# Optimization experiments

Measured on AMD Instinct MI355X. Metric: run time of the kernel, lower is better.

The kernel has to match this reference:

```python
import jax, jax.numpy as jnp
import numpy as np

S, B, D, F = 2048, 8, 1024, 4096
EPS = 1e-5

def setup_inputs() -> dict:
    key = jax.random.key(0)
    ks = jax.random.split(key, 16)
    sc = lambda fan_in: 1.0 / np.sqrt(fan_in)
    inp = {
        'src': jax.random.normal(ks[0], (S, B, D), dtype=jnp.float32),
        'wq': jax.random.uniform(ks[1], (D, D), jnp.float32, -sc(D), sc(D)),
        'bq': jnp.zeros((D,), jnp.float32),
        'wk': jax.random.uniform(ks[2], (D, D), jnp.float32, -sc(D), sc(D)),
        'bk': jnp.zeros((D,), jnp.float32),
        'wv': jax.random.uniform(ks[3], (D, D), jnp.float32, -sc(D), sc(D)),
        'bv': jnp.zeros((D,), jnp.float32),
        'wo': jax.random.uniform(ks[4], (D, D), jnp.float32, -sc(D), sc(D)),
        'bo': jnp.zeros((D,), jnp.float32),
        'w1': jax.random.uniform(ks[5], (F, D), jnp.float32, -sc(D), sc(D)),
        'b1': jnp.zeros((F,), jnp.float32),
        'w2': jax.random.uniform(ks[6], (D, F), jnp.float32, -sc(F), sc(F)),
        'b2': jnp.zeros((D,), jnp.float32),
        'g1': jnp.ones((D,), jnp.float32),
        'be1': jnp.zeros((D,), jnp.float32),
        'g2': jnp.ones((D,), jnp.float32),
        'be2': jnp.zeros((D,), jnp.float32),
    }
    return inp

def _layer_norm(x, g, b):
    mu = jnp.mean(x, axis=-1, keepdims=True)
    var = jnp.mean(jnp.square(x - mu), axis=-1, keepdims=True)
    return (x - mu) / jnp.sqrt(var + EPS) * g + b

def _forward(src, wq, bq, wk, bk, wv, bv, wo, bo, w1, b1, w2, b2, g1, be1, g2, be2):
    # Linear attention (ELU+1 feature map, no normalizer — faithful to source)
    Q = jax.nn.elu(src @ wq.T + bq) + 1.0  # [S,B,D]
    K = jax.nn.elu(src @ wk.T + bk) + 1.0  # [S,B,D]
    V = src @ wv.T + bv                    # [S,B,D]
    KV = jnp.einsum('sbd,sbe->bde', K, V)  # [B,D,D]
    attn = jnp.einsum('sbd,bde->sbe', Q, KV)  # [S,B,D]
    attn = attn @ wo.T + bo
    x = _layer_norm(src + attn, g1, be1)   # dropout is identity (p=0 / eval)
    ffn = jax.nn.relu(x @ w1.T + b1) @ w2.T + b2
    return _layer_norm(x + ffn, g2, be2)

def reference(src, wq, bq, wk, bk, wv, bv, wo, bo, w1, b1, w2, b2, g1, be1, g2, be2):
    return _forward(src, wq, bq, wk, bk, wv, bv, wo, bo, w1, b1, w2, b2, g1, be1, g2, be2)
```

## Files before the change

kernel.cpp:

```cpp
#include <hip/hip_runtime.h>
#include <hip/hip_bf16.h>
#include <math.h>


typedef __attribute__((ext_vector_type(8))) short short8;
typedef __attribute__((ext_vector_type(4))) short short4_t;
typedef __attribute__((ext_vector_type(4))) float f32x4;

#define S_DIM 2048
#define B_DIM 8
#define D_DIM 1024
#define F_DIM 4096

__device__ __forceinline__ unsigned short f2bf(float f) {
  __hip_bfloat16 h = __float2bfloat16(f);
  return *reinterpret_cast<unsigned short*>(&h);
}

#define GLD16(gp, sp)                                              \
  __builtin_amdgcn_global_load_lds(                                \
      (const __attribute__((address_space(1))) void*)(gp),         \
      (__attribute__((address_space(3))) void*)(sp), 16, 0, 0)

#define BAR()                                  \
  do {                                         \
    asm volatile("" ::: "memory");             \
    __builtin_amdgcn_s_barrier();              \
    asm volatile("" ::: "memory");             \
  } while (0)
#define WAITVM6() asm volatile("s_waitcnt vmcnt(6)" ::: "memory")
#define WAITVM10() asm volatile("s_waitcnt vmcnt(10)" ::: "memory")
#define WAITVM0() asm volatile("s_waitcnt vmcnt(0)" ::: "memory")
#define LGKM0_FENCE()                                        \
  do {                                                       \
    asm volatile("s_waitcnt lgkmcnt(0)" ::: "memory");       \
    __builtin_amdgcn_sched_barrier(0);                       \
  } while (0)

template <int EPI>
__global__ __launch_bounds__(512, 2) void gemm256_kernel(
    const unsigned short* __restrict__ A, long lda, long sA,
    const unsigned short* __restrict__ B, long ldb, long sB,
    void* __restrict__ Cv, long ldc, long sC,
    const float* __restrict__ bias,
    const float* __restrict__ resid, long ldr, long sR, int K) {
  __shared__ short lds[65536];
  const int gx = gridDim.x;
  const int nwg = gx * gridDim.y;
  const int orig = blockIdx.y * gx + blockIdx.x;
  const int cpx = nwg >> 3;
  const int wgid = (orig & 7) * cpx + (orig >> 3);
  const int bx = wgid % gx, by = wgid / gx;
  const int bz = blockIdx.z;
  const unsigned short* Ablk = A + (long)bz * sA + (long)by * 256 * lda;
  const unsigned short* Bblk = B + (long)bz * sB + (long)bx * 256 * ldb;

  const int tid = threadIdx.x;
  const int w = tid >> 6, lane = tid & 63;
  const int wm = w >> 2, wn = w & 3;
  const int lr = lane & 15, kh = lane >> 4;

  const int sr = w * 8 + (lane >> 3);
  const int sc = ((lane & 7) ^ (lane >> 3)) * 8;
  const int br0 = sr + ((sr >> 5) << 5);
  const unsigned short* pA = Ablk + (long)sr * lda + sc;
  const unsigned short* pB = Bblk + (long)br0 * ldb + sc;
  const long dA1 = 128 * lda, dAh = 64 * lda;
  const long dB1 = 128 * ldb, dBh = 32 * ldb;
  const int dst0 = w * 1024;
  const int dst1 = (8 + w) * 1024;

#define STAGE_A(bufOff, h, rel)                                               \
  do {                                                                        \
    GLD16(pA + (h) * dAh + (rel) * 64,                                        \
          (char*)lds + (bufOff) + (h)*16384 + dst0);                          \
    GLD16(pA + (h) * dAh + dA1 + (rel) * 64,                                  \
          (char*)lds + (bufOff) + (h)*16384 + dst1);                          \
  } while (0)
#define STAGE_B(bufOff, nh, rel)                                              \
  do {                                                                        \
    GLD16(pB + (nh) * dBh + (rel) * 64,                                       \
          (char*)lds + (bufOff) + 32768 + (nh)*16384 + dst0);                 \
    GLD16(pB + (nh) * dBh + dB1 + (rel) * 64,                                 \
          (char*)lds + (bufOff) + 32768 + (nh)*16384 + dst1);                 \
  } while (0)

  const int chk0 = ((kh ^ (lr & 7)) << 4);
  const int chk1 = (((4 + kh) ^ (lr & 7)) << 4);
  const int aRdBase = (wm * 64 + lr) * 128;
  const int bRdBase = (wn * 32 + lr) * 128;

  short8 af[4][2], b0r[2][2], b1r[2][2];
  f32x4 acc[8][4];
#pragma unroll
  for (int m = 0; m < 8; ++m)
#pragma unroll
    for (int n = 0; n < 4; ++n)
#pragma unroll
      for (int j = 0; j < 4; ++j) acc[m][n][j] = 0.f;

#define LDA_H(bufOff, h)                                                     \
  do {                                                                       \
    const char* _p = (const char*)lds + (bufOff) + (h)*16384 + aRdBase;      \
    _Pragma("unroll") for (int m = 0; m < 4; ++m) {                          \
      af[m][0] = *(const short8*)(_p + m * 2048 + chk0);                     \
      af[m][1] = *(const short8*)(_p + m * 2048 + chk1);                     \
    }                                                                        \
  } while (0)
#define LDB_H(dst, bufOff, nh)                                               \
  do {                                                                       \
    const char* _p = (const char*)lds + (bufOff) + 32768 + (nh)*16384 + bRdBase; \
    _Pragma("unroll") for (int n = 0; n < 2; ++n) {                          \
      dst[n][0] = *(const short8*)(_p + n * 2048 + chk0);                    \
      dst[n][1] = *(const short8*)(_p + n * 2048 + chk1);                    \
    }                                                                        \
  } while (0)
#define MFMA_Q(mh, nh, bset)                                                 \
  do {                                                                       \
    __builtin_amdgcn_s_setprio(1);                                           \
    _Pragma("unroll") for (int m = 0; m < 4; ++m)                            \
    _Pragma("unroll") for (int n = 0; n < 2; ++n)                            \
    _Pragma("unroll") for (int ks = 0; ks < 2; ++ks)                         \
      acc[(mh)*4 + m][(nh)*2 + n] = __builtin_amdgcn_mfma_f32_16x16x32_bf16( \
          af[m][ks], bset[n][ks], acc[(mh)*4 + m][(nh)*2 + n], 0, 0, 0);     \
    __builtin_amdgcn_s_setprio(0);                                           \
  } while (0)

  const int T = K >> 6;
  STAGE_A(0, 0, 0); STAGE_B(0, 0, 0); STAGE_B(0, 1, 0); STAGE_A(0, 1, 0);
  STAGE_A(65536, 0, 1); STAGE_B(65536, 0, 1); STAGE_B(65536, 1, 1);
  WAITVM10(); BAR();
  LDB_H(b0r, 0, 0);

  for (int i = 0; i < (T >> 1) - 1; ++i) {
    LDA_H(0, 0); STAGE_A(65536, 1, 1);
    BAR(); LGKM0_FENCE(); MFMA_Q(0, 0, b0r); BAR();
    LDB_H(b1r, 0, 1); STAGE_A(0, 0, 2);
    BAR(); LGKM0_FENCE(); MFMA_Q(0, 1, b1r); BAR();
    LDA_H(0, 1); STAGE_B(0, 0, 2);
    BAR(); LGKM0_FENCE(); MFMA_Q(1, 1, b1r); BAR();
    STAGE_B(0, 1, 2);
    WAITVM6(); BAR(); MFMA_Q(1, 0, b0r); LDB_H(b0r, 65536, 0); BAR();
    LDA_H(65536, 0); STAGE_A(0, 1, 2);
    BAR(); LGKM0_FENCE(); MFMA_Q(0, 0, b0r); BAR();
    LDB_H(b1r, 65536, 1); STAGE_A(65536, 0, 3);
    BAR(); LGKM0_FENCE(); MFMA_Q(0, 1, b1r); BAR();
    LDA_H(65536, 1); STAGE_B(65536, 0, 3);
    BAR(); LGKM0_FENCE(); MFMA_Q(1, 1, b1r); BAR();
    STAGE_B(65536, 1, 3);
    WAITVM6(); BAR(); MFMA_Q(1, 0, b0r); LDB_H(b0r, 0, 0); BAR();
    pA += 128; pB += 128;
  }

  LDA_H(0, 0); STAGE_A(65536, 1, 1);
  BAR(); LGKM0_FENCE(); MFMA_Q(0, 0, b0r); BAR();
  LDB_H(b1r, 0, 1);
  BAR(); LGKM0_FENCE(); MFMA_Q(0, 1, b1r); BAR();
  LDA_H(0, 1);
  BAR(); LGKM0_FENCE(); MFMA_Q(1, 1, b1r); BAR();
  WAITVM0(); BAR(); MFMA_Q(1, 0, b0r); LDB_H(b0r, 65536, 0); BAR();
  LDA_H(65536, 0);
  BAR(); LGKM0_FENCE(); MFMA_Q(0, 0, b0r); BAR();
  LDB_H(b1r, 65536, 1);
  BAR(); LGKM0_FENCE(); MFMA_Q(0, 1, b1r); BAR();
  LDA_H(65536, 1);
  BAR(); LGKM0_FENCE(); MFMA_Q(1, 1, b1r); BAR();
  LGKM0_FENCE(); MFMA_Q(1, 0, b0r);

  const long gm0 = (long)by * 256 + wm * 128;
  const long gn0 = (long)bx * 256 + wn * 64;
  if constexpr (EPI == 4) {
    float* C = (float*)Cv + (long)bz * sC;
    const float* R = resid + (long)bz * sR;
#pragma unroll
    for (int mg = 0; mg < 8; ++mg)
#pragma unroll
      for (int ng = 0; ng < 4; ++ng) {
        const long col = gn0 + ng * 16 + lr;
        const float bcol = bias[col];
#pragma unroll
        for (int j = 0; j < 4; ++j) {
          const long row = gm0 + mg * 16 + kh * 4 + j;
          C[row * ldc + col] = acc[mg][ng][j] + bcol + R[row * ldr + col];
        }
      }
  } else {
    unsigned short* C = (unsigned short*)Cv + (long)bz * sC;
    const bool do_elu = (EPI == 5) && (gn0 < 2048);
#pragma unroll
    for (int mg = 0; mg < 8; ++mg)
#pragma unroll
      for (int ng = 0; ng < 4; ++ng) {
        const long col = gn0 + ng * 16 + lr;
        const float bcol = bias[col];
#pragma unroll
        for (int j = 0; j < 4; ++j) {
          const long row = gm0 + mg * 16 + kh * 4 + j;
          float v = acc[mg][ng][j] + bcol;
          if constexpr (EPI == 3) v = fmaxf(v, 0.f);
          if constexpr (EPI == 5) {
            if (do_elu) v = (v > 0.f) ? (v + 1.f) : expf(v);
          }
          C[row * ldc + col] = f2bf(v);
        }
      }
  }
#undef STAGE_A
#undef STAGE_B
#undef LDA_H
#undef LDB_H
#undef MFMA_Q
}

template <int EPI>
__global__ __launch_bounds__(256, 2) void gemm_bt_kernel(
    const unsigned short* __restrict__ A, long lda, long sA,
    const unsigned short* __restrict__ B, long ldb, long sB,
    void* __restrict__ Cv, long ldc, long sC,
    const float* __restrict__ bias,
    const float* __restrict__ resid, long ldr, long sR, int K) {
  __shared__ short As[128 * 32];
  __shared__ short Bs[128 * 32];
  const int gx = gridDim.x;
  const int nwg = gx * gridDim.y;
  const int orig = blockIdx.y * gx + blockIdx.x;
  const int cpx = nwg >> 3;
  const int wgid = (orig & 7) * cpx + (orig >> 3);
  const int bx = wgid % gx;
  const int by = wgid / gx;

  const int bz = blockIdx.z;
  const unsigned short* Ab = A + (long)bz * sA + (long)by * 128 * lda;
  const unsigned short* Bb = B + (long)bz * sB + (long)bx * 128 * ldb;
  const int tid = threadIdx.x;
  const int w = tid >> 6, lane = tid & 63;
  const int srow = lane >> 2;
  const int scol = (lane & 3) * 8;
  const int wr = (w >> 1) * 64, wc = (w & 1) * 64;
  const int lr = lane & 15, kh = lane >> 4;

  f32x4 acc[4][4];
#pragma unroll
  for (int m = 0; m < 4; ++m)
#pragma unroll
    for (int n = 0; n < 4; ++n)
#pragma unroll
      for (int j = 0; j < 4; ++j) acc[m][n][j] = 0.f;

  const unsigned short* ga0 = Ab + (long)(w * 16 + srow) * lda + scol;
  const unsigned short* ga1 = Ab + (long)(64 + w * 16 + srow) * lda + scol;
  const unsigned short* gb0 = Bb + (long)(w * 16 + srow) * ldb + scol;
  const unsigned short* gb1 = Bb + (long)(64 + w * 16 + srow) * ldb + scol;
  short* la0 = &As[(w * 16) * 32];
  short* la1 = &As[(64 + w * 16) * 32];
  short* lb0 = &Bs[(w * 16) * 32];
  short* lb1 = &Bs[(64 + w * 16) * 32];

  for (int k0 = 0; k0 < K; k0 += 32) {
    GLD16(ga0 + k0, la0);
    GLD16(ga1 + k0, la1);
    GLD16(gb0 + k0, lb0);
    GLD16(gb1 + k0, lb1);
    __syncthreads();
    short8 af[4], bf[4];
#pragma unroll
    for (int m = 0; m < 4; ++m)
      af[m] = *(const short8*)&As[(wr + m * 16 + lr) * 32 + kh * 8];
#pragma unroll
    for (int n = 0; n < 4; ++n)
      bf[n] = *(const short8*)&Bs[(wc + n * 16 + lr) * 32 + kh * 8];
#pragma unroll
    for (int m = 0; m < 4; ++m)
#pragma unroll
      for (int n = 0; n < 4; ++n)
        acc[m][n] =
            __builtin_amdgcn_mfma_f32_16x16x32_bf16(af[m], bf[n], acc[m][n], 0, 0, 0);
    __syncthreads();
  }

  const long gm0 = (long)by * 128 + wr;
  const long gn0 = (long)bx * 128 + wc;
  unsigned short* C = (unsigned short*)Cv + (long)bz * sC;
#pragma unroll
  for (int m = 0; m < 4; ++m)
#pragma unroll
    for (int n = 0; n < 4; ++n) {
      const long col = gn0 + n * 16 + lr;
#pragma unroll
      for (int j = 0; j < 4; ++j) {
        const long row = gm0 + m * 16 + kh * 4 + j;
        C[row * ldc + col] = f2bf(acc[m][n][j]);
      }
    }
}

__global__ __launch_bounds__(256) void transpose_kernel(
    const unsigned short* __restrict__ in, unsigned short* __restrict__ out,
    long ld) {
  __shared__ unsigned short t[64][68];
  const int b = blockIdx.z;
  const long s0 = (long)blockIdx.x * 64, d0 = (long)blockIdx.y * 64;
  const int tid = threadIdx.x;
  {
    const int r = tid >> 3, c = (tid & 7) * 8;
#pragma unroll
    for (int it = 0; it < 2; ++it) {
      const int s = r + it * 32;
      const unsigned short* g = &in[((s0 + s) * B_DIM + b) * ld + d0 + c];
      short4_t v0 = *(const short4_t*)g;
      short4_t v1 = *(const short4_t*)(g + 4);
      *(short4_t*)&t[s][c] = v0;
      *(short4_t*)&t[s][c + 4] = v1;
    }
  }
  __syncthreads();
  {
    const int d = tid >> 3, c = (tid & 7) * 8;
#pragma unroll
    for (int it = 0; it < 2; ++it) {
      const int dd = d + it * 32;
      short8 v;
#pragma unroll
      for (int j = 0; j < 8; ++j) v[j] = (short)t[c + j][dd];
      *(short8*)&out[(long)b * ((long)D_DIM * S_DIM) + (d0 + dd) * S_DIM + s0 + c] = v;
    }
  }
}

template <int WRITE_BF16>
__global__ __launch_bounds__(256) void layernorm_kernel(
    const float* in, float* outf, unsigned short* __restrict__ outb,
    const float* __restrict__ gamma, const float* __restrict__ beta) {
  const long row = blockIdx.x;
  const float* x = in + row * D_DIM;
  const int tid = threadIdx.x;
  const int lane = tid & 63, w = tid >> 6;
  f32x4 v = *(const f32x4*)&x[tid * 4];
  float s = v[0] + v[1] + v[2] + v[3];
  float q = v[0] * v[0] + v[1] * v[1] + v[2] * v[2] + v[3] * v[3];
#pragma unroll
  for (int off = 32; off > 0; off >>= 1) {
    s += __shfl_down(s, off, 64);
    q += __shfl_down(q, off, 64);
  }
  __shared__ float red[8];
  if (lane == 0) { red[w] = s; red[w + 4] = q; }
  __syncthreads();
  s = red[0] + red[1] + red[2] + red[3];
  q = red[4] + red[5] + red[6] + red[7];
  const float mu = s * (1.f / D_DIM);
  const float var = q * (1.f / D_DIM) - mu * mu;
  const float rs = rsqrtf(var + 1e-5f);
  f32x4 g = *(const f32x4*)&gamma[tid * 4];
  f32x4 bb = *(const f32x4*)&beta[tid * 4];
  f32x4 o;
#pragma unroll
  for (int j = 0; j < 4; ++j) o[j] = (v[j] - mu) * rs * g[j] + bb[j];
  *(f32x4*)&outf[row * D_DIM + tid * 4] = o;
  if constexpr (WRITE_BF16) {
    short4_t ob;
#pragma unroll
    for (int j = 0; j < 4; ++j) ob[j] = (short)f2bf(o[j]);
    *(short4_t*)&outb[row * D_DIM + tid * 4] = ob;
  }
}

__global__ __launch_bounds__(256) void cast_kernel(
    const float* __restrict__ in, unsigned short* __restrict__ out, long n) {
  long i = ((long)blockIdx.x * 256 + threadIdx.x) * 8;
  if (i >= n) return;
  f32x4 a = *(const f32x4*)&in[i];
  f32x4 b = *(const f32x4*)&in[i + 4];
  short8 v;
#pragma unroll
  for (int j = 0; j < 4; ++j) v[j] = (short)f2bf(a[j]);
#pragma unroll
  for (int j = 0; j < 4; ++j) v[4 + j] = (short)f2bf(b[j]);
  *(short8*)&out[i] = v;
}

extern "C" void kernel_launch(void* const* d_in, const int* in_sizes, int n_in,
                              void* d_out, int out_size, void* d_ws, size_t ws_size,
                              hipStream_t stream) {
  const float* src = (const float*)d_in[0];
  const float* wq  = (const float*)d_in[1];
  const float* bq  = (const float*)d_in[2];
  const float* wk  = (const float*)d_in[3];
  const float* bk  = (const float*)d_in[4];
  const float* wv  = (const float*)d_in[5];
  const float* bv  = (const float*)d_in[6];
  const float* wo  = (const float*)d_in[7];
  const float* bo  = (const float*)d_in[8];
  const float* w1  = (const float*)d_in[9];
  const float* b1  = (const float*)d_in[10];
  const float* w2  = (const float*)d_in[11];
  const float* b2  = (const float*)d_in[12];
  const float* g1  = (const float*)d_in[13];
  const float* be1 = (const float*)d_in[14];
  const float* g2  = (const float*)d_in[15];
  const float* be2 = (const float*)d_in[16];

  const long MB = 1024L * 1024L;
  if (ws_size < 248 * MB) return;
  char* ws = (char*)d_ws;
  unsigned short* w1b   = (unsigned short*)(ws + 0 * MB);
  unsigned short* w2b   = (unsigned short*)(ws + 8 * MB);
  unsigned short* srcb  = (unsigned short*)(ws + 16 * MB);
  unsigned short* Kt    = (unsigned short*)(ws + 16 * MB);
  unsigned short* Vt    = (unsigned short*)(ws + 48 * MB);
  float*          AO    = (float*)(ws + 16 * MB);
  float*          X     = (float*)(ws + 16 * MB);
  unsigned short* KVm   = (unsigned short*)(ws + 80 * MB);
  unsigned short* Mt    = (unsigned short*)(ws + 96 * MB);
  unsigned short* Xb    = (unsigned short*)(ws + 80 * MB);
  unsigned short* wqkvb = (unsigned short*)(ws + 112 * MB);
  float*          bqkv  = (float*)(ws + 118 * MB);
  unsigned short* wob   = (unsigned short*)(ws + 119 * MB);
  unsigned short* QKVb  = (unsigned short*)(ws + 144 * MB);
  unsigned short* H     = (unsigned short*)(ws + 112 * MB);

  const dim3 blk(256);
  const dim3 blk512(512);
  cast_kernel<<<dim3(512), blk, 0, stream>>>(wq, wqkvb, 1048576);
  cast_kernel<<<dim3(512), blk, 0, stream>>>(wk, wqkvb + 1048576, 1048576);
  cast_kernel<<<dim3(512), blk, 0, stream>>>(wv, wqkvb + 2097152, 1048576);
  cast_kernel<<<dim3(512), blk, 0, stream>>>(wo, wob, 1048576);
  cast_kernel<<<dim3(2048), blk, 0, stream>>>(w1, w1b, 4194304);
  cast_kernel<<<dim3(2048), blk, 0, stream>>>(w2, w2b, 4194304);
  cast_kernel<<<dim3(8192), blk, 0, stream>>>(src, srcb, 16777216);
  hipMemcpyAsync(bqkv, bq, 4096, hipMemcpyDeviceToDevice, stream);
  hipMemcpyAsync(bqkv + 1024, bk, 4096, hipMemcpyDeviceToDevice, stream);
  hipMemcpyAsync(bqkv + 2048, bv, 4096, hipMemcpyDeviceToDevice, stream);

  gemm256_kernel<5><<<dim3(12, 64, 1), blk512, 0, stream>>>(
      srcb, 1024, 0, wqkvb, 1024, 0, QKVb, 3072, 0, bqkv, nullptr, 0, 0, 1024);

  transpose_kernel<<<dim3(32, 16, 8), blk, 0, stream>>>(QKVb + 1024, Kt, 3072);
  transpose_kernel<<<dim3(32, 16, 8), blk, 0, stream>>>(QKVb + 2048, Vt, 3072);

  gemm_bt_kernel<0><<<dim3(8, 8, 8), blk, 0, stream>>>(
      Kt, 2048, 2097152, Vt, 2048, 2097152, KVm, 1024, 1048576,
      nullptr, nullptr, 0, 0, 2048);
  gemm_bt_kernel<0><<<dim3(8, 8, 8), blk, 0, stream>>>(
      wob, 1024, 0, KVm, 1024, 1048576, Mt, 1024, 1048576,
      nullptr, nullptr, 0, 0, 1024);
  gemm256_kernel<4><<<dim3(4, 8, 8), blk512, 0, stream>>>(
      QKVb, 24576, 3072, Mt, 1024, 1048576, AO, 8192, 1024,
      bo, src, 8192, 1024, 1024);

  layernorm_kernel<1><<<dim3(16384), blk, 0, stream>>>(AO, X, Xb, g1, be1);

  gemm256_kernel<3><<<dim3(16, 64, 1), blk512, 0, stream>>>(
      Xb, 1024, 0, w1b, 1024, 0, H, 4096, 0, b1, nullptr, 0, 0, 1024);
  gemm256_kernel<4><<<dim3(4, 64, 1), blk512, 0, stream>>>(
      H, 4096, 0, w2b, 4096, 0, (float*)d_out, 1024, 0,
      b2, X, 1024, 0, 4096);

  layernorm_kernel<0><<<dim3(16384), blk, 0, stream>>>(
      (float*)d_out, (float*)d_out, nullptr, g2, be2);
}
```

Measured before the change: 650.6 us.

## Use bf16 intermediates for attention output and LN1, and big-tile GEMMs for KV

The attention output projection now writes bf16 instead of fp32, and a new bf16 layernorm kernel writes only a bf16 normalized activation. The FFN2 epilogue reads that bf16 tensor as its residual in place of the fp32 copy. This cuts memory traffic for the intermediates. The two batched KV GEMMs move from the 128-tile kernel to the 256-tile 512-thread kernel, and the old kernel is deleted. The trade-off is lower precision in the residual path and fewer workgroups (128) for the KV GEMMs.

```diff
diff --git a/kernel.cpp b/kernel.cpp
--- a/kernel.cpp
+++ b/kernel.cpp
@@ -15,6 +15,9 @@
 __device__ __forceinline__ unsigned short f2bf(float f) {
   __hip_bfloat16 h = __float2bfloat16(f);
   return *reinterpret_cast<unsigned short*>(&h);
+}
+__device__ __forceinline__ float bf2f(unsigned short u) {
+  return __bfloat162float(*reinterpret_cast<const __hip_bfloat16*>(&u));
 }
 
 #define GLD16(gp, sp)                                              \
@@ -43,7 +46,7 @@
     const unsigned short* __restrict__ B, long ldb, long sB,
     void* __restrict__ Cv, long ldc, long sC,
     const float* __restrict__ bias,
-    const float* __restrict__ resid, long ldr, long sR, int K) {
+    const void* __restrict__ residv, long ldr, long sR, int K) {
   __shared__ short lds[65536];
   const int gx = gridDim.x;
   const int nwg = gx * gridDim.y;
@@ -169,9 +172,9 @@
 
   const long gm0 = (long)by * 256 + wm * 128;
   const long gn0 = (long)bx * 256 + wn * 64;
-  if constexpr (EPI == 4) {
+  if constexpr (EPI == 6) {
     float* C = (float*)Cv + (long)bz * sC;
-    const float* R = resid + (long)bz * sR;
+    const unsigned short* R = (const unsigned short*)residv + (long)bz * sR;
 #pragma unroll
     for (int mg = 0; mg < 8; ++mg)
 #pragma unroll
@@ -181,7 +184,22 @@
 #pragma unroll
         for (int j = 0; j < 4; ++j) {
           const long row = gm0 + mg * 16 + kh * 4 + j;
-          C[row * ldc + col] = acc[mg][ng][j] + bcol + R[row * ldr + col];
+          C[row * ldc + col] = acc[mg][ng][j] + bcol + bf2f(R[row * ldr + col]);
+        }
+      }
+  } else if constexpr (EPI == 7) {
+    unsigned short* C = (unsigned short*)Cv + (long)bz * sC;
+    const float* R = (const float*)residv + (long)bz * sR;
+#pragma unroll
+    for (int mg = 0; mg < 8; ++mg)
+#pragma unroll
+      for (int ng = 0; ng < 4; ++ng) {
+        const long col = gn0 + ng * 16 + lr;
+        const float bcol = bias[col];
+#pragma unroll
+        for (int j = 0; j < 4; ++j) {
+          const long row = gm0 + mg * 16 + kh * 4 + j;
+          C[row * ldc + col] = f2bf(acc[mg][ng][j] + bcol + R[row * ldr + col]);
         }
       }
   } else {
@@ -192,7 +210,8 @@
 #pragma unroll
       for (int ng = 0; ng < 4; ++ng) {
         const long col = gn0 + ng * 16 + lr;
-        const float bcol = bias[col];
+        float bcol = 0.f;
+        if constexpr (EPI != 0) bcol = bias[col];
 #pragma unroll
         for (int j = 0; j < 4; ++j) {
           const long row = gm0 + mg * 16 + kh * 4 + j;
@@ -212,88 +231,6 @@
 #undef MFMA_Q
 }
 
-template <int EPI>
-__global__ __launch_bounds__(256, 2) void gemm_bt_kernel(
-    const unsigned short* __restrict__ A, long lda, long sA,
-    const unsigned short* __restrict__ B, long ldb, long sB,
-    void* __restrict__ Cv, long ldc, long sC,
-    const float* __restrict__ bias,
-    const float* __restrict__ resid, long ldr, long sR, int K) {
-  __shared__ short As[128 * 32];
-  __shared__ short Bs[128 * 32];
-  const int gx = gridDim.x;
-  const int nwg = gx * gridDim.y;
-  const int orig = blockIdx.y * gx + blockIdx.x;
-  const int cpx = nwg >> 3;
-  const int wgid = (orig & 7) * cpx + (orig >> 3);
-  const int bx = wgid % gx;
-  const int by = wgid / gx;
-
-  const int bz = blockIdx.z;
-  const unsigned short* Ab = A + (long)bz * sA + (long)by * 128 * lda;
-  const unsigned short* Bb = B + (long)bz * sB + (long)bx * 128 * ldb;
-  const int tid = threadIdx.x;
-  const int w = tid >> 6, lane = tid & 63;
-  const int srow = lane >> 2;
-  const int scol = (lane & 3) * 8;
-  const int wr = (w >> 1) * 64, wc = (w & 1) * 64;
-  const int lr = lane & 15, kh = lane >> 4;
-
-  f32x4 acc[4][4];
-#pragma unroll
-  for (int m = 0; m < 4; ++m)
-#pragma unroll
-    for (int n = 0; n < 4; ++n)
-#pragma unroll
-      for (int j = 0; j < 4; ++j) acc[m][n][j] = 0.f;
-
-  const unsigned short* ga0 = Ab + (long)(w * 16 + srow) * lda + scol;
-  const unsigned short* ga1 = Ab + (long)(64 + w * 16 + srow) * lda + scol;
-  const unsigned short* gb0 = Bb + (long)(w * 16 + srow) * ldb + scol;
-  const unsigned short* gb1 = Bb + (long)(64 + w * 16 + srow) * ldb + scol;
-  short* la0 = &As[(w * 16) * 32];
-  short* la1 = &As[(64 + w * 16) * 32];
-  short* lb0 = &Bs[(w * 16) * 32];
-  short* lb1 = &Bs[(64 + w * 16) * 32];
-
-  for (int k0 = 0; k0 < K; k0 += 32) {
-    GLD16(ga0 + k0, la0);
-    GLD16(ga1 + k0, la1);
-    GLD16(gb0 + k0, lb0);
-    GLD16(gb1 + k0, lb1);
-    __syncthreads();
-    short8 af[4], bf[4];
-#pragma unroll
-    for (int m = 0; m < 4; ++m)
-      af[m] = *(const short8*)&As[(wr + m * 16 + lr) * 32 + kh * 8];
-#pragma unroll
-    for (int n = 0; n < 4; ++n)
-      bf[n] = *(const short8*)&Bs[(wc + n * 16 + lr) * 32 + kh * 8];
-#pragma unroll
-    for (int m = 0; m < 4; ++m)
-#pragma unroll
-      for (int n = 0; n < 4; ++n)
-        acc[m][n] =
-            __builtin_amdgcn_mfma_f32_16x16x32_bf16(af[m], bf[n], acc[m][n], 0, 0, 0);
-    __syncthreads();
-  }
-
-  const long gm0 = (long)by * 128 + wr;
-  const long gn0 = (long)bx * 128 + wc;
-  unsigned short* C = (unsigned short*)Cv + (long)bz * sC;
-#pragma unroll
-  for (int m = 0; m < 4; ++m)
-#pragma unroll
-    for (int n = 0; n < 4; ++n) {
-      const long col = gn0 + n * 16 + lr;
-#pragma unroll
-      for (int j = 0; j < 4; ++j) {
-        const long row = gm0 + m * 16 + kh * 4 + j;
-        C[row * ldc + col] = f2bf(acc[m][n][j]);
-      }
-    }
-}
-
 __global__ __launch_bounds__(256) void transpose_kernel(
     const unsigned short* __restrict__ in, unsigned short* __restrict__ out,
     long ld) {
@@ -327,9 +264,8 @@
   }
 }
 
-template <int WRITE_BF16>
 __global__ __launch_bounds__(256) void layernorm_kernel(
-    const float* in, float* outf, unsigned short* __restrict__ outb,
+    const float* in, float* outf,
     const float* __restrict__ gamma, const float* __restrict__ beta) {
   const long row = blockIdx.x;
   const float* x = in + row * D_DIM;
@@ -357,12 +293,40 @@
 #pragma unroll
   for (int j = 0; j < 4; ++j) o[j] = (v[j] - mu) * rs * g[j] + bb[j];
   *(f32x4*)&outf[row * D_DIM + tid * 4] = o;
-  if constexpr (WRITE_BF16) {
-    short4_t ob;
-#pragma unroll
-    for (int j = 0; j < 4; ++j) ob[j] = (short)f2bf(o[j]);
-    *(short4_t*)&outb[row * D_DIM + tid * 4] = ob;
-  }
+}
+
+__global__ __launch_bounds__(256) void layernorm_bf_kernel(
+    const unsigned short* __restrict__ in, unsigned short* __restrict__ out,
+    const float* __restrict__ gamma, const float* __restrict__ beta) {
+  const long row = blockIdx.x;
+  const int tid = threadIdx.x;
+  const int lane = tid & 63, w = tid >> 6;
+  short4_t r4 = *(const short4_t*)&in[row * D_DIM + tid * 4];
+  f32x4 v;
+#pragma unroll
+  for (int j = 0; j < 4; ++j) v[j] = bf2f((unsigned short)r4[j]);
+  float s = v[0] + v[1] + v[2] + v[3];
+  float q = v[0] * v[0] + v[1] * v[1] + v[2] * v[2] + v[3] * v[3];
+#pragma unroll
+  for (int off = 32; off > 0; off >>= 1) {
+    s += __shfl_down(s, off, 64);
+    q += __shfl_down(q, off, 64);
+  }
+  __shared__ float red[8];
+  if (lane == 0) { red[w] = s; red[w + 4] = q; }
+  __syncthreads();
+  s = red[0] + red[1] + red[2] + red[3];
+  q = red[4] + red[5] + red[6] + red[7];
+  const float mu = s * (1.f / D_DIM);
+  const float var = q * (1.f / D_DIM) - mu * mu;
+  const float rs = rsqrtf(var + 1e-5f);
+  f32x4 g = *(const f32x4*)&gamma[tid * 4];
+  f32x4 bb = *(const f32x4*)&beta[tid * 4];
+  short4_t ob;
+#pragma unroll
+  for (int j = 0; j < 4; ++j)
+    ob[j] = (short)f2bf((v[j] - mu) * rs * g[j] + bb[j]);
+  *(short4_t*)&out[row * D_DIM + tid * 4] = ob;
 }
 
 __global__ __launch_bounds__(256) void cast_kernel(
@@ -407,12 +371,11 @@
   unsigned short* w2b   = (unsigned short*)(ws + 8 * MB);
   unsigned short* srcb  = (unsigned short*)(ws + 16 * MB);
   unsigned short* Kt    = (unsigned short*)(ws + 16 * MB);
+  unsigned short* AOb   = (unsigned short*)(ws + 16 * MB);
   unsigned short* Vt    = (unsigned short*)(ws + 48 * MB);
-  float*          AO    = (float*)(ws + 16 * MB);
-  float*          X     = (float*)(ws + 16 * MB);
+  unsigned short* Xb    = (unsigned short*)(ws + 48 * MB);
   unsigned short* KVm   = (unsigned short*)(ws + 80 * MB);
   unsigned short* Mt    = (unsigned short*)(ws + 96 * MB);
-  unsigned short* Xb    = (unsigned short*)(ws + 80 * MB);
   unsigned short* wqkvb = (unsigned short*)(ws + 112 * MB);
   float*          bqkv  = (float*)(ws + 118 * MB);
   unsigned short* wob   = (unsigned short*)(ws + 119 * MB);
@@ -438,24 +401,24 @@
   transpose_kernel<<<dim3(32, 16, 8), blk, 0, stream>>>(QKVb + 1024, Kt, 3072);
   transpose_kernel<<<dim3(32, 16, 8), blk, 0, stream>>>(QKVb + 2048, Vt, 3072);
 
-  gemm_bt_kernel<0><<<dim3(8, 8, 8), blk, 0, stream>>>(
+  gemm256_kernel<0><<<dim3(4, 4, 8), blk512, 0, stream>>>(
       Kt, 2048, 2097152, Vt, 2048, 2097152, KVm, 1024, 1048576,
       nullptr, nullptr, 0, 0, 2048);
-  gemm_bt_kernel<0><<<dim3(8, 8, 8), blk, 0, stream>>>(
+  gemm256_kernel<0><<<dim3(4, 4, 8), blk512, 0, stream>>>(
       wob, 1024, 0, KVm, 1024, 1048576, Mt, 1024, 1048576,
       nullptr, nullptr, 0, 0, 1024);
-  gemm256_kernel<4><<<dim3(4, 8, 8), blk512, 0, stream>>>(
-      QKVb, 24576, 3072, Mt, 1024, 1048576, AO, 8192, 1024,
+  gemm256_kernel<7><<<dim3(4, 8, 8), blk512, 0, stream>>>(
+      QKVb, 24576, 3072, Mt, 1024, 1048576, AOb, 8192, 1024,
       bo, src, 8192, 1024, 1024);
 
-  layernorm_kernel<1><<<dim3(16384), blk, 0, stream>>>(AO, X, Xb, g1, be1);
+  layernorm_bf_kernel<<<dim3(16384), blk, 0, stream>>>(AOb, Xb, g1, be1);
 
   gemm256_kernel<3><<<dim3(16, 64, 1), blk512, 0, stream>>>(
       Xb, 1024, 0, w1b, 1024, 0, H, 4096, 0, b1, nullptr, 0, 0, 1024);
-  gemm256_kernel<4><<<dim3(4, 64, 1), blk512, 0, stream>>>(
+  gemm256_kernel<6><<<dim3(4, 64, 1), blk512, 0, stream>>>(
       H, 4096, 0, w2b, 4096, 0, (float*)d_out, 1024, 0,
-      b2, X, 1024, 0, 4096);
-
-  layernorm_kernel<0><<<dim3(16384), blk, 0, stream>>>(
-      (float*)d_out, (float*)d_out, nullptr, g2, be2);
-}
+      b2, Xb, 1024, 0, 4096);
+
+  layernorm_kernel<<<dim3(16384), blk, 0, stream>>>(
+      (float*)d_out, (float*)d_out, g2, be2);
+}
```

After: 626.5 us. 1.04x faster.
